# Kernel optimization log

Measured on AMD Instinct MI355X. Metric: run time of the kernel, lower is better.

## Reference

```python
import jax, jax.numpy as jnp
import numpy as np
import math

B, Hs, Ws, C, NH, PP = 4, 32, 32, 1024, 16, 128
N = Hs * Ws
HD = C // NH
MAX_REL = 32
ROPE_THETA = 10000.0


def _gelu(t):
    return jax.nn.gelu(t, approximate=False)  # torch nn.GELU default (erf)


def _rope(x):
    # x: [B, nh, N, hd]; interleaved even/odd rotation as in _apply_rope
    hd = x.shape[-1]
    inv_freq = 1.0 / (ROPE_THETA ** (jnp.arange(0, hd, 2, dtype=jnp.float32) / hd))
    pos = jnp.arange(x.shape[-2], dtype=jnp.float32)
    ang = pos[:, None] * inv_freq[None, :]  # [N, hd/2]
    sin, cos = jnp.sin(ang), jnp.cos(ang)
    x1, x2 = x[..., 0::2], x[..., 1::2]
    return jnp.stack([x1 * cos - x2 * sin, x2 * cos + x1 * sin], axis=-1).reshape(x.shape)


def _rel_bias(table):
    # static index computation (numpy), gather from learned table -> [1, NH, N, N]
    coords = np.arange(Hs)
    cy, cx = np.meshgrid(coords, coords, indexing='ij')
    cf = np.stack([cy.reshape(-1), cx.reshape(-1)])  # [2, N]
    rel = cf[:, :, None] - cf[:, None, :]            # [2, N, N]
    idx = (rel[0] + MAX_REL - 1) * (2 * MAX_REL - 1) + (rel[1] + MAX_REL - 1)
    return table[jnp.asarray(idx.reshape(-1))].reshape(N, N, NH).transpose(2, 0, 1)[None]


def setup_inputs() -> dict:
    key = jax.random.key(0)
    ks = iter(jax.random.split(key, 40))
    def w(shape, s=0.02):
        return jax.random.normal(next(ks), shape, jnp.float32) * s
    return dict(
        x=jax.random.normal(next(ks), (B, N, C), jnp.float32),
        plucker=jax.random.normal(next(ks), (B, Hs, Ws, 6), jnp.float32),
        w_qkv=w((C, 3 * C)), w_self_proj=w((C, C)), b_self_proj=jnp.zeros((C,), jnp.float32),
        pl_w1=w((6, 2 * PP)), pl_b1=jnp.zeros((2 * PP,), jnp.float32),
        pl_w2=w((2 * PP, PP)), pl_b2=jnp.zeros((PP,), jnp.float32),
        pl_w3=w((PP, PP)), pl_b3=jnp.zeros((PP,), jnp.float32),
        w_cq=w((C, C)), w_pk=w((PP, C)), w_pv=w((PP, C)),
        w_cross_proj=w((C, C)), b_cross_proj=jnp.zeros((C,), jnp.float32),
        ray_dir_bias=w((NH,)),
        ds_w1=w((6, 4 * NH)), ds_b1=jnp.zeros((4 * NH,), jnp.float32),
        ds_w2=w((4 * NH, NH)), ds_b2=jnp.zeros((NH,), jnp.float32),
        gb_w1=w((2 * PP, C // 2)), gb_b1=jnp.zeros((C // 2,), jnp.float32),
        gb_w2=w((C // 2, NH)), gb_b2=jnp.zeros((NH,), jnp.float32),
        rel_table=w(((2 * MAX_REL - 1) ** 2, NH)),
        gfe_w1=w((C + PP, C)), gfe_b1=jnp.zeros((C,), jnp.float32),
        gfe_w2=w((C, C)), gfe_b2=jnp.zeros((C,), jnp.float32),
    )


def reference(x, plucker, w_qkv, w_self_proj, b_self_proj,
              pl_w1, pl_b1, pl_w2, pl_b2, pl_w3, pl_b3,
              w_cq, w_pk, w_pv, w_cross_proj, b_cross_proj,
              ray_dir_bias, ds_w1, ds_b1, ds_w2, ds_b2,
              gb_w1, gb_b1, gb_w2, gb_b2, rel_table,
              gfe_w1, gfe_b1, gfe_w2, gfe_b2):
    scale = HD ** (-0.5)
    pl_flat = plucker.reshape(B, N, 6)

    # ---- self attention with RoPE + relative position bias ----
    qkv = (x @ w_qkv).reshape(B, N, 3, NH, HD).transpose(2, 0, 3, 1, 4)
    q, k, v = qkv[0], qkv[1], qkv[2]          # [B, NH, N, HD]
    q, k = _rope(q), _rope(k)
    attn = jnp.einsum('bhnd,bhmd->bhnm', q, k) * scale + _rel_bias(rel_table)
    attn = jax.nn.softmax(attn, axis=-1)
    sa = jnp.einsum('bhnm,bhmd->bhnd', attn, v).transpose(0, 2, 1, 3).reshape(B, N, C)
    sa = sa @ w_self_proj + b_self_proj

    # ---- plucker mlp embedding ----
    pp = _gelu(pl_flat @ pl_w1 + pl_b1)
    pp = _gelu(pp @ pl_w2 + pl_b2)
    pp = pp @ pl_w3 + pl_b3                   # [B, N, PP]

    # ---- cross attention (features -> plucker) with geometric biases ----
    cq = (sa @ w_cq).reshape(B, N, NH, HD).transpose(0, 2, 1, 3)
    ck = (pp @ w_pk).reshape(B, N, NH, HD).transpose(0, 2, 1, 3)
    cv = (pp @ w_pv).reshape(B, N, NH, HD).transpose(0, 2, 1, 3)
    cq, ck = _rope(cq), _rope(ck)
    ca = jnp.einsum('bhnd,bhmd->bhnm', cq, ck) * scale

    # ray direction similarity bias (per-head learned weight)
    d = pl_flat[..., :3]
    dn = d / jnp.maximum(jnp.linalg.norm(d, axis=-1, keepdims=True), 1e-12)
    sim = jnp.einsum('bnd,bmd->bnm', dn, dn)  # [B, N, N]
    ca = ca + sim[:, None, :, :] * ray_dir_bias[None, :, None, None]

    # distance-aware per-query multiplicative scale
    ds = jnp.tanh(_gelu(pl_flat @ ds_w1 + ds_b1) @ ds_w2 + ds_b2)  # [B, N, NH]
    ca = ca * (1.0 + ds.transpose(0, 2, 1)[..., None])

    # geometric attention bias from spatial diffs of plucker features
    p2 = pp.reshape(B, Hs, Ws, PP)
    hdiff = jnp.pad(jnp.abs(p2[:, :, 1:] - p2[:, :, :-1]), ((0, 0), (0, 0), (0, 1), (0, 0)))
    vdiff = jnp.pad(jnp.abs(p2[:, 1:] - p2[:, :-1]), ((0, 0), (0, 1), (0, 0), (0, 0)))
    sd = jnp.concatenate([hdiff, vdiff], axis=-1).reshape(B, N, 2 * PP)
    gb = jnp.tanh(_gelu(sd @ gb_w1 + gb_b1) @ gb_w2 + gb_b2)  # [B, N, NH]
    ca = ca + gb.transpose(0, 2, 1)[:, :, None, :]            # broadcast over queries

    ca = jax.nn.softmax(ca, axis=-1)
    co = jnp.einsum('bhnm,bhmd->bhnd', ca, cv).transpose(0, 2, 1, 3).reshape(B, N, C)
    co = co @ w_cross_proj + b_cross_proj

    # ---- geometric feature enhancement + residual ----
    enh = _gelu(jnp.concatenate([co, pp], axis=-1) @ gfe_w1 + gfe_b1) @ gfe_w2 + gfe_b2
    return enh + x
```

## Files before the change

kernel.cpp:

```cpp
#include <hip/hip_runtime.h>
#include <math.h>

#define B_ 4
#define N_ 1024
#define C_ 1024
#define NH_ 16
#define HD_ 64
#define PP_ 128
#define LOG2E 1.4426950408889634f

typedef __bf16 bf16;
typedef __attribute__((ext_vector_type(8))) __bf16 bf16x8;
typedef __attribute__((ext_vector_type(4))) __bf16 bf16x4;
typedef __attribute__((ext_vector_type(4))) float f32x4;

#define MFMA_BF16(a, b, c) __builtin_amdgcn_mfma_f32_16x16x32_bf16((a), (b), (c), 0, 0, 0)

__device__ __forceinline__ float gelu_f(float x) {
    return 0.5f * x * (1.0f + erff(x * 0.70710678118654752f));
}

__device__ __forceinline__ void gload16(const void* g, void* l) {
    __builtin_amdgcn_global_load_lds(
        (const __attribute__((address_space(1))) void*)g,
        (__attribute__((address_space(3))) void*)l, 16, 0, 0);
}

__device__ __forceinline__ void stage64(const bf16* __restrict__ g, int pitchB,
                                        bf16* lds, int t) {
    int row = t >> 3, c = t & 7;
    const char* src = (const char*)g + (size_t)row * pitchB + ((c ^ (row & 7)) << 4);
    gload16(src, lds + (size_t)(t & 448) * 8);
}

__device__ __forceinline__ void stage64e(const bf16* __restrict__ g, bf16* lds, int t) {
    if (t < 256) {
        int row = t >> 2, c = t & 3;
        const char* src = (const char*)g + (size_t)row * 64 + ((c ^ (row & 3)) << 4);
        gload16(src, lds + (size_t)(t & 192) * 8);
    }
}

__device__ __forceinline__ bf16x8 lds8_swz(const bf16* lds, int row, int colb) {
    return *reinterpret_cast<const bf16x8*>(
        (const char*)lds + row * 128 + (colb ^ ((row & 7) << 4)));
}

__device__ __forceinline__ bf16x8 lds8_swz64(const bf16* lds, int row, int cb) {
    return *reinterpret_cast<const bf16x8*>(
        (const char*)lds + row * 64 + (((cb >> 4) ^ (row & 3)) << 4));
}

__global__ __launch_bounds__(256) void rope_tab_k(float2* __restrict__ rt)
{
    int g = blockIdx.x * 256 + threadIdx.x;
    const int n = g >> 5, i = g & 31;
    const float inv = powf(10000.0f, -(float)(2 * i) / 64.0f);
    const float ang = (float)n * inv;
    rt[g] = make_float2(cosf(ang), sinf(ang));
}

__global__ __launch_bounds__(256) void relT_k(const float* __restrict__ rel_table,
                                              float* __restrict__ relT)
{
    int g = blockIdx.x * 256 + threadIdx.x;
    if (g >= 16 * 3969) return;
    int h = g / 3969, idx = g - h * 3969;
    relT[g] = rel_table[idx * 16 + h];
}

struct TJobs {
    const float* src[11];
    bf16* dst[11];
    int K[11];
    int N[11];
};

__global__ __launch_bounds__(256) void tcast_k(TJobs J)
{
    const int j = blockIdx.z;
    const int Kd = J.K[j], Nd = J.N[j];
    const int n0 = blockIdx.x * 32, k0 = blockIdx.y * 32;
    if (n0 >= Nd || k0 >= Kd) return;
    __shared__ float tl[32][33];
    const int t = threadIdx.x, tx = t & 31, ty = t >> 5;
    const float* src = J.src[j];
    bf16* dst = J.dst[j];
    #pragma unroll
    for (int r = 0; r < 4; ++r) {
        int kk = ty + r * 8;
        tl[kk][tx] = src[(size_t)(k0 + kk) * Nd + n0 + tx];
    }
    __syncthreads();
    #pragma unroll
    for (int r = 0; r < 4; ++r) {
        int nn = ty + r * 8;
        dst[(size_t)(n0 + nn) * Kd + k0 + tx] = (bf16)tl[tx][nn];
    }
}

__global__ __launch_bounds__(256) void cast_rm(const float* __restrict__ in,
                                               bf16* __restrict__ out, int n4)
{
    int g = blockIdx.x * 256 + threadIdx.x;
    if (g >= n4) return;
    float4 v = reinterpret_cast<const float4*>(in)[g];
    bf16x4 o = {(bf16)v.x, (bf16)v.y, (bf16)v.z, (bf16)v.w};
    reinterpret_cast<bf16x4*>(out)[g] = o;
}

template<int NI, int BK>
__global__ __launch_bounds__(256) void gemm_m(
    const bf16* __restrict__ A, const bf16* __restrict__ A2,
    const bf16* __restrict__ Bt, const bf16* __restrict__ Bt2,
    const float* __restrict__ bias, const float* __restrict__ resid,
    void* __restrict__ out0, void* __restrict__ out1, void* __restrict__ out2,
    const float2* __restrict__ rtab,
    int M, int N, int K, int K1A, int K1B, int epi, int act_gelu, float scale)
{
    __shared__ bf16 As[2][128 * BK];
    __shared__ bf16 Bs[2][NI * 32 * BK];
    const int t = threadIdx.x;
    const int w = t >> 6, lane = t & 63;
    const int row0 = blockIdx.y * 128, col0 = blockIdx.x * (NI * 32);
    const int wm = w >> 1, wn = w & 1;
    const int K2A = K - K1A, K2B = K - K1B;
    f32x4 acc[4][NI];
    #pragma unroll
    for (int mi = 0; mi < 4; ++mi)
        #pragma unroll
        for (int ni = 0; ni < NI; ++ni)
            acc[mi][ni] = (f32x4){0.f, 0.f, 0.f, 0.f};

    #define STAGE_AB32(k0, buf)                                                \
        {                                                                      \
            _Pragma("unroll")                                                  \
            for (int r = 0; r < 2; ++r) {                                      \
                int c = r * 256 + t;                                           \
                int rr = c >> 2, koff = (c & 3) * 8;                           \
                const bf16* srca = ((k0) < K1A)                                \
                    ? A + (size_t)(row0 + rr) * K1A + (k0) + koff              \
                    : A2 + (size_t)(row0 + rr) * K2A + ((k0) - K1A) + koff;    \
                gload16(srca, As[buf] + (size_t)(r * 256 + (t & 192)) * 8);    \
            }                                                                  \
            _Pragma("unroll")                                                  \
            for (int r = 0; r < NI / 2; ++r) {                                 \
                int c = r * 256 + t;                                           \
                int rr = c >> 2, koff = (c & 3) * 8;                           \
                const bf16* srcb = ((k0) < K1B)                                \
                    ? Bt + (size_t)(col0 + rr) * K1B + (k0) + koff             \
                    : Bt2 + (size_t)(col0 + rr) * K2B + ((k0) - K1B) + koff;   \
                gload16(srcb, Bs[buf] + (size_t)(r * 256 + (t & 192)) * 8);    \
            }                                                                  \
        }

    #define STAGE_AB64(k0, buf)                                                \
        {                                                                      \
            const bf16* abase; int apitch;                                     \
            if ((k0) < K1A) { abase = A + (k0); apitch = K1A; }                \
            else            { abase = A2 + ((k0) - K1A); apitch = K2A; }       \
            _Pragma("unroll")                                                  \
            for (int r = 0; r < 4; ++r) {                                      \
                int c = r * 256 + t;                                           \
                int rr = c >> 3, cc = c & 7;                                   \
                const char* srca = (const char*)(abase + (size_t)(row0 + rr) * apitch) \
                                   + ((cc ^ (rr & 7)) << 4);                   \
                gload16(srca, As[buf] + (size_t)(r * 256 + (t & 192)) * 8);    \
            }                                                                  \
            const bf16* bbase; int bpitch;                                     \
            if ((k0) < K1B) { bbase = Bt + (k0); bpitch = K1B; }               \
            else            { bbase = Bt2 + ((k0) - K1B); bpitch = K2B; }      \
            _Pragma("unroll")                                                  \
            for (int r = 0; r < NI; ++r) {                                     \
                int c = r * 256 + t;                                           \
                int rr = c >> 3, cc = c & 7;                                   \
                const char* srcb = (const char*)(bbase + (size_t)(col0 + rr) * bpitch) \
                                   + ((cc ^ (rr & 7)) << 4);                   \
                gload16(srcb, Bs[buf] + (size_t)(r * 256 + (t & 192)) * 8);    \
            }                                                                  \
        }

    int cur = 0;
    const int nk = K / BK;
    if constexpr (BK == 32) {
        STAGE_AB32(0, 0);
        __syncthreads();
        for (int kk = 0; kk < nk; ++kk) {
            if (kk + 1 < nk) STAGE_AB32((kk + 1) * 32, cur ^ 1);
            bf16x8 af[4], bfv[NI];
            #pragma unroll
            for (int mi = 0; mi < 4; ++mi)
                af[mi] = *reinterpret_cast<const bf16x8*>(
                    As[cur] + (wm * 64 + mi * 16 + (lane & 15)) * 32 + (lane >> 4) * 8);
            #pragma unroll
            for (int ni = 0; ni < NI; ++ni)
                bfv[ni] = *reinterpret_cast<const bf16x8*>(
                    Bs[cur] + (wn * (NI * 16) + ni * 16 + (lane & 15)) * 32 + (lane >> 4) * 8);
            #pragma unroll
            for (int mi = 0; mi < 4; ++mi)
                #pragma unroll
                for (int ni = 0; ni < NI; ++ni)
                    acc[mi][ni] = MFMA_BF16(af[mi], bfv[ni], acc[mi][ni]);
            __syncthreads();
            cur ^= 1;
        }
    } else {
        STAGE_AB64(0, 0);
        __syncthreads();
        for (int kk = 0; kk < nk; ++kk) {
            if (kk + 1 < nk) STAGE_AB64((kk + 1) * 64, cur ^ 1);
            bf16x8 af[4][2], bfv[NI][2];
            #pragma unroll
            for (int mi = 0; mi < 4; ++mi)
                #pragma unroll
                for (int kh = 0; kh < 2; ++kh)
                    af[mi][kh] = lds8_swz(As[cur], wm * 64 + mi * 16 + (lane & 15),
                                          kh * 64 + (lane >> 4) * 16);
            #pragma unroll
            for (int ni = 0; ni < NI; ++ni)
                #pragma unroll
                for (int kh = 0; kh < 2; ++kh)
                    bfv[ni][kh] = lds8_swz(Bs[cur], wn * (NI * 16) + ni * 16 + (lane & 15),
                                           kh * 64 + (lane >> 4) * 16);
            #pragma unroll
            for (int kh = 0; kh < 2; ++kh)
                #pragma unroll
                for (int mi = 0; mi < 4; ++mi)
                    #pragma unroll
                    for (int ni = 0; ni < NI; ++ni)
                        acc[mi][ni] = MFMA_BF16(af[mi][kh], bfv[ni][kh], acc[mi][ni]);
            __syncthreads();
            cur ^= 1;
        }
    }
    #undef STAGE_AB32
    #undef STAGE_AB64

    #pragma unroll
    for (int mi = 0; mi < 4; ++mi) {
        #pragma unroll
        for (int ni = 0; ni < NI; ++ni) {
            const int col = col0 + wn * (NI * 16) + ni * 16 + (lane & 15);
            if (epi <= 1 || epi == 5) {
                const float bv = bias ? bias[col] : 0.f;
                #pragma unroll
                for (int j = 0; j < 4; ++j) {
                    const int row = row0 + wm * 64 + mi * 16 + (lane >> 4) * 4 + j;
                    float v = acc[mi][ni][j] + bv;
                    if (act_gelu) v = gelu_f(v);
                    if (epi == 0) {
                        if (resid) v += resid[(size_t)row * N + col];
                        ((float*)out0)[(size_t)row * N + col] = v;
                    } else if (epi == 1) {
                        ((bf16*)out0)[(size_t)row * N + col] = (bf16)v;
                    } else {
                        ((float*)out0)[(size_t)row * N + col] = v;
                        ((bf16*)out1)[(size_t)row * N + col] = (bf16)v;
                    }
                }
            } else if (epi == 2) {
                const int reg = col >> 10;
                const int h = (col >> 6) & 15, d = col & 63;
                if (reg <= 1) {
                    bf16* dst = reg == 0 ? (bf16*)out0 : (bf16*)out1;
                    const float sc = reg == 0 ? scale : 1.0f;
                    #pragma unroll
                    for (int j = 0; j < 4; ++j) {
                        const int row = row0 + wm * 64 + mi * 16 + (lane >> 4) * 4 + j;
                        const int b = row >> 10, n = row & 1023;
                        float v = acc[mi][ni][j];
                        float pv = __shfl_xor(v, 1);
                        float2 cs = rtab[(n << 5) + (d >> 1)];
                        float o = (d & 1) == 0 ? v * cs.x - pv * cs.y
                                               : v * cs.x + pv * cs.y;
                        dst[((size_t)((b * 16 + h) * 1024 + n)) * 64 + d] = (bf16)(o * sc);
                    }
                } else {
                    bf16x4 o4;
                    #pragma unroll
                    for (int j = 0; j < 4; ++j) o4[j] = (bf16)acc[mi][ni][j];
                    const int row = row0 + wm * 64 + mi * 16 + (lane >> 4) * 4;
                    const int b = row >> 10, n = row & 1023;
                    *reinterpret_cast<bf16x4*>(
                        (bf16*)out2 + ((size_t)((b * 16 + h) * 64 + d)) * 1024 + n) = o4;
                }
            } else if (epi == 3 || epi == 6) {
                const int h = (col >> 6) & 15, d = col & 63;
                #pragma unroll
                for (int j = 0; j < 4; ++j) {
                    const int row = row0 + wm * 64 + mi * 16 + (lane >> 4) * 4 + j;
                    const int b = row >> 10, n = row & 1023;
                    float v = acc[mi][ni][j];
                    float pv = __shfl_xor(v, 1);
                    float2 cs = rtab[(n << 5) + (d >> 1)];
                    float o = (d & 1) == 0 ? v * cs.x - pv * cs.y
                                           : v * cs.x + pv * cs.y;
                    float sc = scale;
                    if (epi == 6) sc *= 1.0f + resid[(size_t)row * 16 + h];
                    ((bf16*)out0)[((size_t)((b * 16 + h) * 1024 + n)) * 64 + d] = (bf16)(o * sc);
                }
            } else {
                const int h = (col >> 6) & 15, d = col & 63;
                bf16x4 o4;
                #pragma unroll
                for (int j = 0; j < 4; ++j) o4[j] = (bf16)acc[mi][ni][j];
                const int row = row0 + wm * 64 + mi * 16 + (lane >> 4) * 4;
                const int b = row >> 10, n = row & 1023;
                *reinterpret_cast<bf16x4*>(
                    (bf16*)out0 + ((size_t)((b * 16 + h) * 64 + d)) * 1024 + n) = o4;
            }
        }
    }
}

__global__ __launch_bounds__(256) void extfill_k(
    const float* __restrict__ dn, const float* __restrict__ ds,
    const float* __restrict__ gb, const float* __restrict__ rdb,
    bf16* __restrict__ qe, bf16* __restrict__ ke)
{
    int g = blockIdx.x * 256 + threadIdx.x;
    if (g >= 65536) return;
    const int bh = g >> 10, n = g & 1023;
    const int b = bh >> 4, h = bh & 15;
    const size_t rn = (size_t)b * 1024 + n;
    const float c1 = rdb[h] * LOG2E * (1.0f + ds[rn * 16 + h]);
    const float dx = dn[rn * 4], dy = dn[rn * 4 + 1], dz = dn[rn * 4 + 2];
    bf16x8 z = {};
    bf16x8 q0 = z, k0 = z;
    q0[0] = (bf16)(dx * c1); q0[1] = (bf16)(dy * c1); q0[2] = (bf16)(dz * c1); q0[3] = (bf16)1.0f;
    k0[0] = (bf16)dx; k0[1] = (bf16)dy; k0[2] = (bf16)dz; k0[3] = (bf16)(gb[rn * 16 + h] * LOG2E);
    bf16x8* qp = reinterpret_cast<bf16x8*>(qe + (size_t)g * 32);
    bf16x8* kp = reinterpret_cast<bf16x8*>(ke + (size_t)g * 32);
    qp[0] = q0; qp[1] = z; qp[2] = z; qp[3] = z;
    kp[0] = k0; kp[1] = z; kp[2] = z; kp[3] = z;
}

__device__ __forceinline__ void attn_bid(int bid, int& bh, int& r0t) {
    const int xcd = bid & 7, s = bid >> 3;
    bh = (s >> 3) * 8 + xcd;
    r0t = s & 7;
}

__global__ __launch_bounds__(512) void attn_self_m(
    const bf16* __restrict__ qb, const bf16* __restrict__ kb, const bf16* __restrict__ vtb,
    const float* __restrict__ relT, bf16* __restrict__ sab)
{
    __shared__ bf16 Ks[2][64 * 64];
    __shared__ bf16 Vs[2][80 * 64];
    __shared__ bf16 Ps[128 * 72];
    __shared__ float relb[2][320];
    const int t = threadIdx.x, w = t >> 6, lane = t & 63;
    int bh, r0t;
    attn_bid(blockIdx.x, bh, r0t);
    const int b = bh >> 4, h = bh & 15, r0 = r0t * 128;
    const float* relTh = relT + h * 3969;
    const int y0 = r0 >> 5;

    {
        const bf16* g = qb + ((size_t)bh * 1024 + r0) * 64;
        #pragma unroll
        for (int r = 0; r < 2; ++r) {
            int i = r * 512 + t;
            int row = i >> 3, c = i & 7;
            const char* src = (const char*)g + (size_t)row * 128 + ((c ^ (row & 7)) << 4);
            gload16(src, Ps + (size_t)(r * 512 + (t & 448)) * 8);
        }
    }
    __syncthreads();
    bf16x8 aq[2];
    {
        const int qr = w * 16 + (lane & 15);
        aq[0] = lds8_swz(Ps, qr, (lane >> 4) * 16);
        aq[1] = lds8_swz(Ps, qr, 64 + (lane >> 4) * 16);
    }
    for (int i = t; i < 2048; i += 512) {
        int buf = i >> 10, idx = i & 1023;
        int row = 64 + (idx >> 6), col = idx & 63;
        Vs[buf][row * 64 + col] = (row == 64) ? (bf16)1.0f : (bf16)0.0f;
    }
    __syncthreads();
    stage64(kb + (size_t)bh * 65536, 128, Ks[0], t);
    stage64(vtb + (size_t)bh * 65536, 2048, Vs[0], t);
    if (t < 320) relb[0][t] = LOG2E * relTh[(y0 + 30 + (t >> 6)) * 63 + min(t & 63, 62)];

    float m_run[4];
    f32x4 of[4], ofe;
    #pragma unroll
    for (int j = 0; j < 4; ++j) m_run[j] = -3e38f;
    #pragma unroll
    for (int dt = 0; dt < 4; ++dt) of[dt] = (f32x4){0.f, 0.f, 0.f, 0.f};
    ofe = (f32x4){0.f, 0.f, 0.f, 0.f};

    const int qrow_lo = (lane >> 4) * 4;
    int dybase[4];
    #pragma unroll
    for (int j = 0; j < 4; ++j) {
        int qg = r0 + w * 16 + qrow_lo + j;
        dybase[j] = (((qg >> 5) - y0) + 1) * 64 + (qg & 31) + 31;
    }
    __syncthreads();

    int cur = 0;
    for (int mt = 0; mt < 16; ++mt) {
        if (mt < 15) {
            stage64(kb + (size_t)bh * 65536 + (size_t)(mt + 1) * 64 * 64, 128, Ks[cur ^ 1], t);
            stage64(vtb + (size_t)bh * 65536 + (size_t)(mt + 1) * 64, 2048, Vs[cur ^ 1], t);
            if (t < 320)
                relb[cur ^ 1][t] = LOG2E * relTh[(y0 - 2 * (mt + 1) + 30 + (t >> 6)) * 63 + min(t & 63, 62)];
        }
        f32x4 sf[4];
        __builtin_amdgcn_s_setprio(1);
        #pragma unroll
        for (int ct = 0; ct < 4; ++ct) {
            const int kr = ct * 16 + (lane & 15);
            f32x4 a = (f32x4){0.f, 0.f, 0.f, 0.f};
            a = MFMA_BF16(aq[0], lds8_swz(Ks[cur], kr, (lane >> 4) * 16), a);
            a = MFMA_BF16(aq[1], lds8_swz(Ks[cur], kr, 64 + (lane >> 4) * 16), a);
            sf[ct] = a;
        }
        __builtin_amdgcn_s_setprio(0);
        float p[4][4], mx[4];
        #pragma unroll
        for (int j = 0; j < 4; ++j) mx[j] = -3e38f;
        #pragma unroll
        for (int ct = 0; ct < 4; ++ct) {
            const int xm = (ct & 1) * 16 + (lane & 15);
            const int ro = (ct >> 1) * 64 + xm;
            #pragma unroll
            for (int j = 0; j < 4; ++j) {
                float s = sf[ct][j] + relb[cur][dybase[j] - ro];
                p[ct][j] = s;
                mx[j] = fmaxf(mx[j], s);
            }
        }
        #pragma unroll
        for (int d = 1; d < 16; d <<= 1)
            #pragma unroll
            for (int j = 0; j < 4; ++j) mx[j] = fmaxf(mx[j], __shfl_xor(mx[j], d));
        bool need = false;
        #pragma unroll
        for (int j = 0; j < 4; ++j) need |= (mx[j] > m_run[j] + 8.0f);
        if (__any(need)) {
            float alpha[4];
            #pragma unroll
            for (int j = 0; j < 4; ++j) {
                float mn = fmaxf(m_run[j], mx[j]);
                alpha[j] = exp2f(m_run[j] - mn);
                m_run[j] = mn;
            }
            #pragma unroll
            for (int dt = 0; dt < 4; ++dt)
                #pragma unroll
                for (int j = 0; j < 4; ++j) of[dt][j] *= alpha[j];
            #pragma unroll
            for (int j = 0; j < 4; ++j) ofe[j] *= alpha[j];
        }
        #pragma unroll
        for (int ct = 0; ct < 4; ++ct)
            #pragma unroll
            for (int j = 0; j < 4; ++j)
                p[ct][j] = exp2f(p[ct][j] - m_run[j]);
        #pragma unroll
        for (int ct = 0; ct < 4; ++ct)
            #pragma unroll
            for (int j = 0; j < 4; ++j)
                Ps[(w * 16 + qrow_lo + j) * 72 + ct * 16 + (lane & 15)] = (bf16)p[ct][j];
        asm volatile("s_waitcnt lgkmcnt(0)" ::: "memory");
        __builtin_amdgcn_sched_barrier(0);
        bf16x8 ap0 = *reinterpret_cast<const bf16x8*>(Ps + (w * 16 + (lane & 15)) * 72 + (lane >> 4) * 8);
        bf16x8 ap1 = *reinterpret_cast<const bf16x8*>(Ps + (w * 16 + (lane & 15)) * 72 + 32 + (lane >> 4) * 8);
        __builtin_amdgcn_s_setprio(1);
        #pragma unroll
        for (int dt = 0; dt < 4; ++dt) {
            const int vr = dt * 16 + (lane & 15);
            of[dt] = MFMA_BF16(ap0, lds8_swz(Vs[cur], vr, (lane >> 4) * 16), of[dt]);
            of[dt] = MFMA_BF16(ap1, lds8_swz(Vs[cur], vr, 64 + (lane >> 4) * 16), of[dt]);
        }
        {
            const int vr = 64 + (lane & 15);
            ofe = MFMA_BF16(ap0, lds8_swz(Vs[cur], vr, (lane >> 4) * 16), ofe);
            ofe = MFMA_BF16(ap1, lds8_swz(Vs[cur], vr, 64 + (lane >> 4) * 16), ofe);
        }
        __builtin_amdgcn_s_setprio(0);
        __syncthreads();
        cur ^= 1;
    }
    float inv[4];
    #pragma unroll
    for (int j = 0; j < 4; ++j) inv[j] = 1.f / __shfl(ofe[j], lane & 48);
    #pragma unroll
    for (int dt = 0; dt < 4; ++dt)
        #pragma unroll
        for (int j = 0; j < 4; ++j)
            sab[((size_t)(b * N_ + r0 + w * 16 + qrow_lo + j)) * C_ + h * 64 + dt * 16 + (lane & 15)] =
                (bf16)(of[dt][j] * inv[j]);
}

__global__ __launch_bounds__(512) void attn_cross_m(
    const bf16* __restrict__ cq, const bf16* __restrict__ qe,
    const bf16* __restrict__ ck, const bf16* __restrict__ ke,
    const bf16* __restrict__ cvt, bf16* __restrict__ cob)
{
    __shared__ bf16 Ks[2][64 * 64];
    __shared__ bf16 Ke[2][64 * 32];
    __shared__ bf16 Vs[2][80 * 64];
    __shared__ bf16 Ps[128 * 72];
    const int t = threadIdx.x, w = t >> 6, lane = t & 63;
    int bh, r0t;
    attn_bid(blockIdx.x, bh, r0t);
    const int b = bh >> 4, h = bh & 15, r0 = r0t * 128;

    {
        const bf16* g = cq + ((size_t)bh * 1024 + r0) * 64;
        #pragma unroll
        for (int r = 0; r < 2; ++r) {
            int i = r * 512 + t;
            int row = i >> 3, c = i & 7;
            const char* src = (const char*)g + (size_t)row * 128 + ((c ^ (row & 7)) << 4);
            gload16(src, Ps + (size_t)(r * 512 + (t & 448)) * 8);
        }
    }
    {
        const bf16* g = qe + ((size_t)bh * 1024 + r0) * 32;
        int row = t >> 2, c = t & 3;
        const char* src = (const char*)g + (size_t)row * 64 + ((c ^ (row & 3)) << 4);
        gload16(src, Ks[0] + (size_t)(t & 448) * 8);
    }
    __syncthreads();
    bf16x8 aq[2], aqe;
    {
        const int qr = w * 16 + (lane & 15);
        aq[0] = lds8_swz(Ps, qr, (lane >> 4) * 16);
        aq[1] = lds8_swz(Ps, qr, 64 + (lane >> 4) * 16);
        aqe = lds8_swz64(Ks[0], qr, (lane >> 4) * 16);
    }
    for (int i = t; i < 2048; i += 512) {
        int buf = i >> 10, idx = i & 1023;
        int row = 64 + (idx >> 6), col = idx & 63;
        Vs[buf][row * 64 + col] = (row == 64) ? (bf16)1.0f : (bf16)0.0f;
    }
    __syncthreads();
    stage64(ck + (size_t)bh * 65536, 128, Ks[0], t);
    stage64e(ke + (size_t)bh * 32768, Ke[0], t);
    stage64(cvt + (size_t)bh * 65536, 2048, Vs[0], t);

    float m_run[4];
    f32x4 of[4], ofe;
    #pragma unroll
    for (int j = 0; j < 4; ++j) m_run[j] = -3e38f;
    #pragma unroll
    for (int dt = 0; dt < 4; ++dt) of[dt] = (f32x4){0.f, 0.f, 0.f, 0.f};
    ofe = (f32x4){0.f, 0.f, 0.f, 0.f};
    const int qrow_lo = (lane >> 4) * 4;
    __syncthreads();

    int cur = 0;
    for (int mt = 0; mt < 16; ++mt) {
        if (mt < 15) {
            stage64(ck + (size_t)bh * 65536 + (size_t)(mt + 1) * 64 * 64, 128, Ks[cur ^ 1], t);
            stage64e(ke + (size_t)bh * 32768 + (size_t)(mt + 1) * 64 * 32, Ke[cur ^ 1], t);
            stage64(cvt + (size_t)bh * 65536 + (size_t)(mt + 1) * 64, 2048, Vs[cur ^ 1], t);
        }
        f32x4 sf[4];
        __builtin_amdgcn_s_setprio(1);
        #pragma unroll
        for (int ct = 0; ct < 4; ++ct) {
            const int kr = ct * 16 + (lane & 15);
            f32x4 a = (f32x4){0.f, 0.f, 0.f, 0.f};
            a = MFMA_BF16(aq[0], lds8_swz(Ks[cur], kr, (lane >> 4) * 16), a);
            a = MFMA_BF16(aq[1], lds8_swz(Ks[cur], kr, 64 + (lane >> 4) * 16), a);
            a = MFMA_BF16(aqe, lds8_swz64(Ke[cur], kr, (lane >> 4) * 16), a);
            sf[ct] = a;
        }
        __builtin_amdgcn_s_setprio(0);
        float mx[4];
        #pragma unroll
        for (int j = 0; j < 4; ++j)
            mx[j] = fmaxf(fmaxf(sf[0][j], sf[1][j]), fmaxf(sf[2][j], sf[3][j]));
        #pragma unroll
        for (int d = 1; d < 16; d <<= 1)
            #pragma unroll
            for (int j = 0; j < 4; ++j) mx[j] = fmaxf(mx[j], __shfl_xor(mx[j], d));
        bool need = false;
        #pragma unroll
        for (int j = 0; j < 4; ++j) need |= (mx[j] > m_run[j] + 8.0f);
        if (__any(need)) {
            float alpha[4];
            #pragma unroll
            for (int j = 0; j < 4; ++j) {
                float mn = fmaxf(m_run[j], mx[j]);
                alpha[j] = exp2f(m_run[j] - mn);
                m_run[j] = mn;
            }
            #pragma unroll
            for (int dt = 0; dt < 4; ++dt)
                #pragma unroll
                for (int j = 0; j < 4; ++j) of[dt][j] *= alpha[j];
            #pragma unroll
            for (int j = 0; j < 4; ++j) ofe[j] *= alpha[j];
        }
        #pragma unroll
        for (int ct = 0; ct < 4; ++ct)
            #pragma unroll
            for (int j = 0; j < 4; ++j)
                sf[ct][j] = exp2f(sf[ct][j] - m_run[j]);
        #pragma unroll
        for (int ct = 0; ct < 4; ++ct)
            #pragma unroll
            for (int j = 0; j < 4; ++j)
                Ps[(w * 16 + qrow_lo + j) * 72 + ct * 16 + (lane & 15)] = (bf16)sf[ct][j];
        asm volatile("s_waitcnt lgkmcnt(0)" ::: "memory");
        __builtin_amdgcn_sched_barrier(0);
        bf16x8 ap0 = *reinterpret_cast<const bf16x8*>(Ps + (w * 16 + (lane & 15)) * 72 + (lane >> 4) * 8);
        bf16x8 ap1 = *reinterpret_cast<const bf16x8*>(Ps + (w * 16 + (lane & 15)) * 72 + 32 + (lane >> 4) * 8);
        __builtin_amdgcn_s_setprio(1);
        #pragma unroll
        for (int dt = 0; dt < 4; ++dt) {
            const int vr = dt * 16 + (lane & 15);
            of[dt] = MFMA_BF16(ap0, lds8_swz(Vs[cur], vr, (lane >> 4) * 16), of[dt]);
            of[dt] = MFMA_BF16(ap1, lds8_swz(Vs[cur], vr, 64 + (lane >> 4) * 16), of[dt]);
        }
        {
            const int vr = 64 + (lane & 15);
            ofe = MFMA_BF16(ap0, lds8_swz(Vs[cur], vr, (lane >> 4) * 16), ofe);
            ofe = MFMA_BF16(ap1, lds8_swz(Vs[cur], vr, 64 + (lane >> 4) * 16), ofe);
        }
        __builtin_amdgcn_s_setprio(0);
        __syncthreads();
        cur ^= 1;
    }
    float inv[4];
    #pragma unroll
    for (int j = 0; j < 4; ++j) inv[j] = 1.f / __shfl(ofe[j], lane & 48);
    #pragma unroll
    for (int dt = 0; dt < 4; ++dt)
        #pragma unroll
        for (int j = 0; j < 4; ++j)
            cob[((size_t)(b * N_ + r0 + w * 16 + qrow_lo + j)) * C_ + h * 64 + dt * 16 + (lane & 15)] =
                (bf16)(of[dt][j] * inv[j]);
}

__global__ __launch_bounds__(256) void plucker1_k(
    const float* __restrict__ pl,
    const float* __restrict__ w1, const float* __restrict__ b1,
    const float* __restrict__ dw1, const float* __restrict__ db1,
    const float* __restrict__ dw2, const float* __restrict__ db2,
    bf16* __restrict__ h1b, float* __restrict__ ds, float* __restrict__ dn)
{
    const int t = threadIdx.x;
    __shared__ float plr[6];
    __shared__ float dh[64];
    #pragma unroll 1
    for (int rr = 0; rr < 4; ++rr) {
        const int row = blockIdx.x * 4 + rr;
        if (t < 6) plr[t] = pl[(size_t)row * 6 + t];
        __syncthreads();
        {
            float a = b1[t];
            #pragma unroll
            for (int j = 0; j < 6; ++j) a = fmaf(plr[j], w1[j * 256 + t], a);
            h1b[(size_t)row * 256 + t] = (bf16)gelu_f(a);
        }
        if (t < 64) {
            float d = db1[t];
            #pragma unroll
            for (int j = 0; j < 6; ++j) d = fmaf(plr[j], dw1[j * 64 + t], d);
            dh[t] = gelu_f(d);
        }
        if (t == 0) {
            float x = plr[0], y = plr[1], z = plr[2];
            float nrm = fmaxf(sqrtf(x * x + y * y + z * z), 1e-12f);
            dn[(size_t)row * 4 + 0] = x / nrm;
            dn[(size_t)row * 4 + 1] = y / nrm;
            dn[(size_t)row * 4 + 2] = z / nrm;
            dn[(size_t)row * 4 + 3] = 0.f;
        }
        __syncthreads();
        if (t < 16) {
            float d = db2[t];
            #pragma unroll 8
            for (int j = 0; j < 64; ++j) d = fmaf(dh[j], dw2[j * 16 + t], d);
            ds[(size_t)row * 16 + t] = tanhf(d);
        }
        __syncthreads();
    }
}

__global__ __launch_bounds__(256) void sd_k(const float* __restrict__ pp, bf16* __restrict__ sd)
{
    int g = blockIdx.x * 256 + threadIdx.x;
    if (g >= B_ * N_ * PP_) return;
    const int c = g & 127;
    const int rown = g >> 7;
    const int n = rown & (N_ - 1);
    const int xx = n & 31, yy = (n >> 5) & 31;
    const float cur = pp[g];
    const float hd = (xx < 31) ? fabsf(pp[g + PP_] - cur) : 0.f;
    const float vd = (yy < 31) ? fabsf(pp[g + 32 * PP_] - cur) : 0.f;
    sd[(size_t)rown * 256 + c] = (bf16)hd;
    sd[(size_t)rown * 256 + 128 + c] = (bf16)vd;
}

__global__ __launch_bounds__(256) void gb2_k(
    const bf16* __restrict__ h, const float* __restrict__ w2,
    const float* __restrict__ b2, float* __restrict__ gbv)
{
    __shared__ float w2s[512 * 16];
    const int t = threadIdx.x;
    for (int i = t; i < 8192; i += 256) w2s[i] = w2[i];
    __syncthreads();
    const int row = blockIdx.x * 16 + (t >> 4);
    const int col = t & 15;
    const bf16* hr = h + (size_t)row * 512;
    float acc = b2[col];
    #pragma unroll 8
    for (int j = 0; j < 512; ++j)
        acc = fmaf((float)hr[j], w2s[j * 16 + col], acc);
    gbv[(size_t)row * 16 + col] = tanhf(acc);
}

extern "C" void kernel_launch(void* const* d_in, const int* in_sizes, int n_in,
                              void* d_out, int out_size, void* d_ws, size_t ws_size,
                              hipStream_t stream)
{
    const float* x     = (const float*)d_in[0];
    const float* pl    = (const float*)d_in[1];
    const float* w_qkv = (const float*)d_in[2];
    const float* w_sp  = (const float*)d_in[3];
    const float* b_sp  = (const float*)d_in[4];
    const float* pl_w1 = (const float*)d_in[5];
    const float* pl_b1 = (const float*)d_in[6];
    const float* pl_w2 = (const float*)d_in[7];
    const float* pl_b2 = (const float*)d_in[8];
    const float* pl_w3 = (const float*)d_in[9];
    const float* pl_b3 = (const float*)d_in[10];
    const float* w_cq  = (const float*)d_in[11];
    const float* w_pk  = (const float*)d_in[12];
    const float* w_pv  = (const float*)d_in[13];
    const float* w_cp  = (const float*)d_in[14];
    const float* b_cp  = (const float*)d_in[15];
    const float* rdb   = (const float*)d_in[16];
    const float* ds_w1 = (const float*)d_in[17];
    const float* ds_b1 = (const float*)d_in[18];
    const float* ds_w2 = (const float*)d_in[19];
    const float* ds_b2 = (const float*)d_in[20];
    const float* gb_w1 = (const float*)d_in[21];
    const float* gb_b1 = (const float*)d_in[22];
    const float* gb_w2 = (const float*)d_in[23];
    const float* gb_b2 = (const float*)d_in[24];
    const float* rel_t = (const float*)d_in[25];
    const float* gfw1  = (const float*)d_in[26];
    const float* gfb1  = (const float*)d_in[27];
    const float* gfw2  = (const float*)d_in[28];
    const float* gfb2  = (const float*)d_in[29];

    char* W = (char*)d_ws;
    float* out = (float*)d_out;
    const size_t MB = 1ull << 20;
    const size_t KB = 1024;

    bf16* qb     = (bf16*)(W + 0);
    bf16* kb     = (bf16*)(W + 8 * MB);
    bf16* vtb    = (bf16*)(W + 16 * MB);
    bf16* cqb    = qb;
    bf16* ckb    = kb;
    bf16* cvtb   = vtb;
    bf16* xb     = (bf16*)(W + 24 * MB);
    bf16* wqkvT  = (bf16*)(W + 32 * MB);
    bf16* wspT   = (bf16*)(W + 38 * MB);
    bf16* wcqT   = (bf16*)(W + 40 * MB);
    bf16* wpkT   = (bf16*)(W + 42 * MB);
    bf16* wpvT   = (bf16*)(W + 42 * MB + 256 * KB);
    bf16* wcpT   = (bf16*)(W + 43 * MB);
    bf16* gfw1T  = (bf16*)(W + 45 * MB);
    bf16* gfw2T  = (bf16*)(W + 48 * MB);
    bf16* plw2T  = (bf16*)(W + 50 * MB);
    bf16* plw3T  = (bf16*)(W + 50 * MB + 64 * KB);
    bf16* gbw1T  = (bf16*)(W + 50 * MB + 128 * KB);
    bf16* sab    = (bf16*)(W + 51 * MB);
    bf16* cob    = sab;
    bf16* sapb   = (bf16*)(W + 59 * MB);
    bf16* copb   = sapb;
    float* pp    = (float*)(W + 67 * MB);
    bf16* ppb    = (bf16*)(W + 69 * MB);
    bf16* sdb16  = (bf16*)(W + 70 * MB);
    bf16* h1b    = (bf16*)(W + 72 * MB);
    bf16* h2b    = (bf16*)(W + 74 * MB);
    bf16* gbh    = (bf16*)(W + 75 * MB);
    float* dsb   = (float*)(W + 79 * MB);
    float* dnb   = (float*)(W + 79 * MB + 256 * KB);
    float* gbb   = (float*)(W + 79 * MB + 320 * KB);
    float2* rtab = (float2*)(W + 80 * MB);
    float* relTb = (float*)(W + 80 * MB + 256 * KB);
    bf16* hidb   = (bf16*)(W + 81 * MB);
    bf16* qeb    = (bf16*)(W + 89 * MB);
    bf16* keb    = (bf16*)(W + 93 * MB);

    const dim3 blk(256);

    TJobs J;
    J.src[0] = w_qkv; J.dst[0] = wqkvT; J.K[0] = 1024; J.N[0] = 3072;
    J.src[1] = w_sp;  J.dst[1] = wspT;  J.K[1] = 1024; J.N[1] = 1024;
    J.src[2] = w_cq;  J.dst[2] = wcqT;  J.K[2] = 1024; J.N[2] = 1024;
    J.src[3] = w_pk;  J.dst[3] = wpkT;  J.K[3] = 128;  J.N[3] = 1024;
    J.src[4] = w_pv;  J.dst[4] = wpvT;  J.K[4] = 128;  J.N[4] = 1024;
    J.src[5] = w_cp;  J.dst[5] = wcpT;  J.K[5] = 1024; J.N[5] = 1024;
    J.src[6] = gfw1;  J.dst[6] = gfw1T; J.K[6] = 1152; J.N[6] = 1024;
    J.src[7] = gfw2;  J.dst[7] = gfw2T; J.K[7] = 1024; J.N[7] = 1024;
    J.src[8] = pl_w2; J.dst[8] = plw2T; J.K[8] = 256;  J.N[8] = 128;
    J.src[9] = pl_w3; J.dst[9] = plw3T; J.K[9] = 128;  J.N[9] = 128;
    J.src[10]= gb_w1; J.dst[10]= gbw1T; J.K[10]= 256;  J.N[10]= 512;
    tcast_k<<<dim3(96, 36, 11), blk, 0, stream>>>(J);
    cast_rm<<<4096, blk, 0, stream>>>(x, xb, 1048576);
    rope_tab_k<<<128, blk, 0, stream>>>(rtab);
    relT_k<<<249, blk, 0, stream>>>(rel_t, relTb);

    gemm_m<4, 32><<<dim3(24, 32), blk, 0, stream>>>(xb, nullptr, wqkvT, nullptr, nullptr, nullptr,
        qb, kb, vtb, rtab, 4096, 3072, 1024, 1024, 1024, 2, 0, 0.125f * LOG2E);
    attn_self_m<<<512, dim3(512), 0, stream>>>(qb, kb, vtb, relTb, sab);
    gemm_m<2, 64><<<dim3(16, 32), blk, 0, stream>>>(sab, nullptr, wspT, nullptr, b_sp, nullptr,
        sapb, nullptr, nullptr, nullptr, 4096, 1024, 1024, 1024, 1024, 1, 0, 1.f);
    plucker1_k<<<1024, blk, 0, stream>>>(pl, pl_w1, pl_b1,
                                         ds_w1, ds_b1, ds_w2, ds_b2, h1b, dsb, dnb);
    gemm_m<2, 64><<<dim3(2, 32), blk, 0, stream>>>(h1b, nullptr, plw2T, nullptr, pl_b2, nullptr,
        h2b, nullptr, nullptr, nullptr, 4096, 128, 256, 256, 256, 1, 1, 1.f);
    gemm_m<2, 64><<<dim3(2, 32), blk, 0, stream>>>(h2b, nullptr, plw3T, nullptr, pl_b3, nullptr,
        pp, ppb, nullptr, nullptr, 4096, 128, 128, 128, 128, 5, 0, 1.f);
    sd_k<<<2048, blk, 0, stream>>>(pp, sdb16);
    gemm_m<2, 64><<<dim3(8, 32), blk, 0, stream>>>(sdb16, nullptr, gbw1T, nullptr, gb_b1, nullptr,
        gbh, nullptr, nullptr, nullptr, 4096, 512, 256, 256, 256, 1, 1, 1.f);
    gb2_k<<<256, blk, 0, stream>>>(gbh, gb_w2, gb_b2, gbb);
    gemm_m<2, 64><<<dim3(16, 32), blk, 0, stream>>>(sapb, nullptr, wcqT, nullptr, nullptr, dsb,
        cqb, nullptr, nullptr, rtab, 4096, 1024, 1024, 1024, 1024, 6, 0, 0.125f * LOG2E);
    gemm_m<2, 64><<<dim3(16, 32), blk, 0, stream>>>(ppb, nullptr, wpkT, nullptr, nullptr, nullptr,
        ckb, nullptr, nullptr, rtab, 4096, 1024, 128, 128, 128, 3, 0, 1.0f);
    gemm_m<2, 64><<<dim3(16, 32), blk, 0, stream>>>(ppb, nullptr, wpvT, nullptr, nullptr, nullptr,
        cvtb, nullptr, nullptr, nullptr, 4096, 1024, 128, 128, 128, 4, 0, 1.f);
    extfill_k<<<256, blk, 0, stream>>>(dnb, dsb, gbb, rdb, qeb, keb);
    attn_cross_m<<<512, dim3(512), 0, stream>>>(cqb, qeb, ckb, keb, cvtb, cob);
    gemm_m<2, 64><<<dim3(16, 32), blk, 0, stream>>>(cob, nullptr, wcpT, nullptr, b_cp, nullptr,
        copb, nullptr, nullptr, nullptr, 4096, 1024, 1024, 1024, 1024, 1, 0, 1.f);
    gemm_m<2, 64><<<dim3(16, 32), blk, 0, stream>>>(copb, ppb, gfw1T, nullptr, gfb1, nullptr,
        hidb, nullptr, nullptr, nullptr, 4096, 1024, 1152, 1024, 1152, 1, 1, 1.f);
    gemm_m<2, 64><<<dim3(16, 32), blk, 0, stream>>>(hidb, nullptr, gfw2T, nullptr, gfb2, x,
        out, nullptr, nullptr, nullptr, 4096, 1024, 1024, 1024, 1024, 0, 0, 1.f);
}
```

Measured before the change: 351.2 us.

## Swizzle P and extra-key LDS tiles, defer row-max shuffle, retile QKV GEMM

Both attention kernels now store the P tile in an XOR-swizzled 128-byte-pitch LDS layout instead of a padded 72-element pitch, and the cross-attention extra-key tile uses a 128-byte swizzled layout with a matching read helper. The cross-lane max reduction is moved inside the rare rescale branch, so the common path skips the shuffles and uses per-lane maxima to decide whether a rescale is needed. The QKV GEMM is switched to a smaller-tile configuration with twice as many blocks. This aims to cut LDS bank conflicts, shuffle overhead and QKV GEMM underutilisation, at the cost of extra address arithmetic and scalar 2-byte swizzled stores.

```diff
diff --git a/kernel.cpp b/kernel.cpp
--- a/kernel.cpp
+++ b/kernel.cpp
@@ -33,10 +33,10 @@
     gload16(src, lds + (size_t)(t & 448) * 8);
 }
 
-__device__ __forceinline__ void stage64e(const bf16* __restrict__ g, bf16* lds, int t) {
+__device__ __forceinline__ void stage32(const bf16* __restrict__ g, bf16* lds, int t) {
     if (t < 256) {
-        int row = t >> 2, c = t & 3;
-        const char* src = (const char*)g + (size_t)row * 64 + ((c ^ (row & 3)) << 4);
+        int row = t >> 3, c = t & 7;
+        const char* src = (const char*)g + (size_t)row * 128 + ((c ^ (row & 7)) << 4);
         gload16(src, lds + (size_t)(t & 192) * 8);
     }
 }
@@ -46,9 +46,10 @@
         (const char*)lds + row * 128 + (colb ^ ((row & 7) << 4)));
 }
 
-__device__ __forceinline__ bf16x8 lds8_swz64(const bf16* lds, int row, int cb) {
-    return *reinterpret_cast<const bf16x8*>(
-        (const char*)lds + row * 64 + (((cb >> 4) ^ (row & 3)) << 4));
+__device__ __forceinline__ bf16x8 lds8_ke(const bf16* lds, int kr, int g) {
+    int r = kr >> 1;
+    int ch = ((kr & 1) * 4 + g) ^ (r & 7);
+    return *reinterpret_cast<const bf16x8*>((const char*)lds + r * 128 + (ch << 4));
 }
 
 __global__ __launch_bounds__(256) void rope_tab_k(float2* __restrict__ rt)
@@ -347,7 +348,7 @@
 {
     __shared__ bf16 Ks[2][64 * 64];
     __shared__ bf16 Vs[2][80 * 64];
-    __shared__ bf16 Ps[128 * 72];
+    __shared__ bf16 Ps[128 * 64];
     __shared__ float relb[2][320];
     const int t = threadIdx.x, w = t >> 6, lane = t & 63;
     int bh, r0t;
@@ -419,9 +420,9 @@
             sf[ct] = a;
         }
         __builtin_amdgcn_s_setprio(0);
-        float p[4][4], mx[4];
-        #pragma unroll
-        for (int j = 0; j < 4; ++j) mx[j] = -3e38f;
+        float p[4][4], lmax[4];
+        #pragma unroll
+        for (int j = 0; j < 4; ++j) lmax[j] = -3e38f;
         #pragma unroll
         for (int ct = 0; ct < 4; ++ct) {
             const int xm = (ct & 1) * 16 + (lane & 15);
@@ -430,18 +431,20 @@
             for (int j = 0; j < 4; ++j) {
                 float s = sf[ct][j] + relb[cur][dybase[j] - ro];
                 p[ct][j] = s;
-                mx[j] = fmaxf(mx[j], s);
+                lmax[j] = fmaxf(lmax[j], s);
             }
         }
-        #pragma unroll
-        for (int d = 1; d < 16; d <<= 1)
-            #pragma unroll
-            for (int j = 0; j < 4; ++j) mx[j] = fmaxf(mx[j], __shfl_xor(mx[j], d));
         bool need = false;
         #pragma unroll
-        for (int j = 0; j < 4; ++j) need |= (mx[j] > m_run[j] + 8.0f);
+        for (int j = 0; j < 4; ++j) need |= (lmax[j] > m_run[j] + 8.0f);
         if (__any(need)) {
-            float alpha[4];
+            float mx[4], alpha[4];
+            #pragma unroll
+            for (int j = 0; j < 4; ++j) mx[j] = lmax[j];
+            #pragma unroll
+            for (int d = 1; d < 16; d <<= 1)
+                #pragma unroll
+                for (int j = 0; j < 4; ++j) mx[j] = fmaxf(mx[j], __shfl_xor(mx[j], d));
             #pragma unroll
             for (int j = 0; j < 4; ++j) {
                 float mn = fmaxf(m_run[j], mx[j]);
@@ -463,12 +466,16 @@
         #pragma unroll
         for (int ct = 0; ct < 4; ++ct)
             #pragma unroll
-            for (int j = 0; j < 4; ++j)
-                Ps[(w * 16 + qrow_lo + j) * 72 + ct * 16 + (lane & 15)] = (bf16)p[ct][j];
+            for (int j = 0; j < 4; ++j) {
+                const int prow = w * 16 + qrow_lo + j;
+                const int ch = (ct * 2 + ((lane & 15) >> 3)) ^ (prow & 7);
+                *reinterpret_cast<bf16*>((char*)Ps + prow * 128 + (ch << 4) + (lane & 7) * 2)
+                    = (bf16)p[ct][j];
+            }
         asm volatile("s_waitcnt lgkmcnt(0)" ::: "memory");
         __builtin_amdgcn_sched_barrier(0);
-        bf16x8 ap0 = *reinterpret_cast<const bf16x8*>(Ps + (w * 16 + (lane & 15)) * 72 + (lane >> 4) * 8);
-        bf16x8 ap1 = *reinterpret_cast<const bf16x8*>(Ps + (w * 16 + (lane & 15)) * 72 + 32 + (lane >> 4) * 8);
+        bf16x8 ap0 = lds8_swz(Ps, w * 16 + (lane & 15), (lane >> 4) * 16);
+        bf16x8 ap1 = lds8_swz(Ps, w * 16 + (lane & 15), 64 + (lane >> 4) * 16);
         __builtin_amdgcn_s_setprio(1);
         #pragma unroll
         for (int dt = 0; dt < 4; ++dt) {
@@ -502,9 +509,9 @@
     const bf16* __restrict__ cvt, bf16* __restrict__ cob)
 {
     __shared__ bf16 Ks[2][64 * 64];
-    __shared__ bf16 Ke[2][64 * 32];
+    __shared__ bf16 Ke[2][32 * 64];
     __shared__ bf16 Vs[2][80 * 64];
-    __shared__ bf16 Ps[128 * 72];
+    __shared__ bf16 Ps[128 * 64];
     const int t = threadIdx.x, w = t >> 6, lane = t & 63;
     int bh, r0t;
     attn_bid(blockIdx.x, bh, r0t);
@@ -520,19 +527,14 @@
             gload16(src, Ps + (size_t)(r * 512 + (t & 448)) * 8);
         }
     }
-    {
-        const bf16* g = qe + ((size_t)bh * 1024 + r0) * 32;
-        int row = t >> 2, c = t & 3;
-        const char* src = (const char*)g + (size_t)row * 64 + ((c ^ (row & 3)) << 4);
-        gload16(src, Ks[0] + (size_t)(t & 448) * 8);
-    }
+    stage64(qe + ((size_t)bh * 1024 + r0) * 32, 128, Ks[0], t);
     __syncthreads();
     bf16x8 aq[2], aqe;
     {
         const int qr = w * 16 + (lane & 15);
         aq[0] = lds8_swz(Ps, qr, (lane >> 4) * 16);
         aq[1] = lds8_swz(Ps, qr, 64 + (lane >> 4) * 16);
-        aqe = lds8_swz64(Ks[0], qr, (lane >> 4) * 16);
+        aqe = lds8_ke(Ks[0], qr, lane >> 4);
     }
     for (int i = t; i < 2048; i += 512) {
         int buf = i >> 10, idx = i & 1023;
@@ -541,7 +543,7 @@
     }
     __syncthreads();
     stage64(ck + (size_t)bh * 65536, 128, Ks[0], t);
-    stage64e(ke + (size_t)bh * 32768, Ke[0], t);
+    stage32(ke + (size_t)bh * 32768, Ke[0], t);
     stage64(cvt + (size_t)bh * 65536, 2048, Vs[0], t);
 
     float m_run[4];
@@ -558,7 +560,7 @@
     for (int mt = 0; mt < 16; ++mt) {
         if (mt < 15) {
             stage64(ck + (size_t)bh * 65536 + (size_t)(mt + 1) * 64 * 64, 128, Ks[cur ^ 1], t);
-            stage64e(ke + (size_t)bh * 32768 + (size_t)(mt + 1) * 64 * 32, Ke[cur ^ 1], t);
+            stage32(ke + (size_t)bh * 32768 + (size_t)(mt + 1) * 64 * 32, Ke[cur ^ 1], t);
             stage64(cvt + (size_t)bh * 65536 + (size_t)(mt + 1) * 64, 2048, Vs[cur ^ 1], t);
         }
         f32x4 sf[4];
@@ -569,23 +571,25 @@
             f32x4 a = (f32x4){0.f, 0.f, 0.f, 0.f};
             a = MFMA_BF16(aq[0], lds8_swz(Ks[cur], kr, (lane >> 4) * 16), a);
             a = MFMA_BF16(aq[1], lds8_swz(Ks[cur], kr, 64 + (lane >> 4) * 16), a);
-            a = MFMA_BF16(aqe, lds8_swz64(Ke[cur], kr, (lane >> 4) * 16), a);
+            a = MFMA_BF16(aqe, lds8_ke(Ke[cur], kr, lane >> 4), a);
             sf[ct] = a;
         }
         __builtin_amdgcn_s_setprio(0);
-        float mx[4];
+        float lmax[4];
         #pragma unroll
         for (int j = 0; j < 4; ++j)
-            mx[j] = fmaxf(fmaxf(sf[0][j], sf[1][j]), fmaxf(sf[2][j], sf[3][j]));
-        #pragma unroll
-        for (int d = 1; d < 16; d <<= 1)
-            #pragma unroll
-            for (int j = 0; j < 4; ++j) mx[j] = fmaxf(mx[j], __shfl_xor(mx[j], d));
+            lmax[j] = fmaxf(fmaxf(sf[0][j], sf[1][j]), fmaxf(sf[2][j], sf[3][j]));
         bool need = false;
         #pragma unroll
-        for (int j = 0; j < 4; ++j) need |= (mx[j] > m_run[j] + 8.0f);
+        for (int j = 0; j < 4; ++j) need |= (lmax[j] > m_run[j] + 8.0f);
         if (__any(need)) {
-            float alpha[4];
+            float mx[4], alpha[4];
+            #pragma unroll
+            for (int j = 0; j < 4; ++j) mx[j] = lmax[j];
+            #pragma unroll
+            for (int d = 1; d < 16; d <<= 1)
+                #pragma unroll
+                for (int j = 0; j < 4; ++j) mx[j] = fmaxf(mx[j], __shfl_xor(mx[j], d));
             #pragma unroll
             for (int j = 0; j < 4; ++j) {
                 float mn = fmaxf(m_run[j], mx[j]);
@@ -607,12 +611,16 @@
         #pragma unroll
         for (int ct = 0; ct < 4; ++ct)
             #pragma unroll
-            for (int j = 0; j < 4; ++j)
-                Ps[(w * 16 + qrow_lo + j) * 72 + ct * 16 + (lane & 15)] = (bf16)sf[ct][j];
+            for (int j = 0; j < 4; ++j) {
+                const int prow = w * 16 + qrow_lo + j;
+                const int ch = (ct * 2 + ((lane & 15) >> 3)) ^ (prow & 7);
+                *reinterpret_cast<bf16*>((char*)Ps + prow * 128 + (ch << 4) + (lane & 7) * 2)
+                    = (bf16)sf[ct][j];
+            }
         asm volatile("s_waitcnt lgkmcnt(0)" ::: "memory");
         __builtin_amdgcn_sched_barrier(0);
-        bf16x8 ap0 = *reinterpret_cast<const bf16x8*>(Ps + (w * 16 + (lane & 15)) * 72 + (lane >> 4) * 8);
-        bf16x8 ap1 = *reinterpret_cast<const bf16x8*>(Ps + (w * 16 + (lane & 15)) * 72 + 32 + (lane >> 4) * 8);
+        bf16x8 ap0 = lds8_swz(Ps, w * 16 + (lane & 15), (lane >> 4) * 16);
+        bf16x8 ap1 = lds8_swz(Ps, w * 16 + (lane & 15), 64 + (lane >> 4) * 16);
         __builtin_amdgcn_s_setprio(1);
         #pragma unroll
         for (int dt = 0; dt < 4; ++dt) {
@@ -815,7 +823,7 @@
     rope_tab_k<<<128, blk, 0, stream>>>(rtab);
     relT_k<<<249, blk, 0, stream>>>(rel_t, relTb);
 
-    gemm_m<4, 32><<<dim3(24, 32), blk, 0, stream>>>(xb, nullptr, wqkvT, nullptr, nullptr, nullptr,
+    gemm_m<2, 64><<<dim3(48, 32), blk, 0, stream>>>(xb, nullptr, wqkvT, nullptr, nullptr, nullptr,
         qb, kb, vtb, rtab, 4096, 3072, 1024, 1024, 1024, 2, 0, 0.125f * LOG2E);
     attn_self_m<<<512, dim3(512), 0, stream>>>(qb, kb, vtb, relTb, sab);
     gemm_m<2, 64><<<dim3(16, 32), blk, 0, stream>>>(sab, nullptr, wspT, nullptr, b_sp, nullptr,
```

Measured after the change: 344.7 us. About the same (-1.8%).
